# Optimization experiments

Measured on AMD Instinct MI355X. Metric: run time of the kernel, lower is better.

Reference implementation:

```python
import jax, jax.numpy as jnp
import numpy as np

N = 8192      # number of nodes (x is [N, N])
S = 2         # number of support (adjacency) matrices
E = 262144    # edges (nnz) per support, avg degree 32
D = 128       # output_dim


def setup_inputs() -> dict:
    key = jax.random.key(0)
    k0, k1, k2, k3, k4 = jax.random.split(key, 5)
    x = jax.random.normal(k0, (N, N), dtype=jnp.float32)
    rows = jax.random.randint(k1, (S, E), 0, N, dtype=jnp.int32)
    cols = jax.random.randint(k2, (S, E), 0, N, dtype=jnp.int32)
    vals = jax.random.uniform(k3, (S, E), dtype=jnp.float32)
    # one glorot [1, D] weight per support; stacked as [S, 1, D]
    w = jax.random.normal(k4, (S, 1, D), dtype=jnp.float32) * 0.05
    return {"x": x, "rows": rows, "cols": cols, "vals": vals, "w": w}


def reference(x, rows, cols, vals, w):
    # x = tf.abs(tf.transpose(x) - x * -1)  ==  |x^T + x|
    x2 = jnp.abs(x.T + x)                      # [N, N]
    # diag(A_s @ x2)[i] = sum_{(i,j) in E_s} A_s[i,j] * x2[j, i]
    contrib = vals * x2[cols, rows]            # [S, E] gather along edges
    diag = jax.vmap(
        lambda r, c: jax.ops.segment_sum(c, r, num_segments=N)
    )(rows, contrib)                           # [S, N]
    # outer product with per-support [1, D] weight, summed over supports
    out = jnp.einsum('sn,sd->nd', diag, w[:, 0, :])  # [N, D]
    return jax.nn.relu(out)
```

## Files before the change

kernel.cpp:

```cpp
#include <hip/hip_runtime.h>


#define N_NODES 8192
#define S_SUP   2
#define E_EDGES 262144
#define D_OUT   128

__global__ void gc_edge_kernel(const float* __restrict__ x,
                               const int*   __restrict__ rows,
                               const int*   __restrict__ cols,
                               const float* __restrict__ vals,
                               float*       __restrict__ diag) {
    int idx = blockIdx.x * blockDim.x + threadIdx.x;
    if (idx >= S_SUP * E_EDGES) return;
    int s = idx >> 18;
    int r = rows[idx];
    int c = cols[idx];
    float v = vals[idx];
    float a = x[(size_t)r * N_NODES + c];
    float b = x[(size_t)c * N_NODES + r];
    float t = fabsf(a + b) * v;
    atomicAdd(&diag[s * N_NODES + r], t);
}

__global__ void gc_out_kernel(const float* __restrict__ diag,
                              const float* __restrict__ w,
                              float*       __restrict__ out) {
    int idx = blockIdx.x * blockDim.x + threadIdx.x;
    int d4 = idx & (D_OUT / 4 - 1);
    int n  = idx >> 5;
    if (n >= N_NODES) return;
    float d0 = diag[n];
    float d1 = diag[N_NODES + n];
    const float4 w0 = ((const float4*)w)[d4];
    const float4 w1 = ((const float4*)w)[D_OUT / 4 + d4];
    float4 o;
    o.x = fmaxf(fmaf(d0, w0.x, d1 * w1.x), 0.0f);
    o.y = fmaxf(fmaf(d0, w0.y, d1 * w1.y), 0.0f);
    o.z = fmaxf(fmaf(d0, w0.z, d1 * w1.z), 0.0f);
    o.w = fmaxf(fmaf(d0, w0.w, d1 * w1.w), 0.0f);
    ((float4*)out)[idx] = o;
}

extern "C" void kernel_launch(void* const* d_in, const int* in_sizes, int n_in,
                              void* d_out, int out_size, void* d_ws, size_t ws_size,
                              hipStream_t stream) {
    const float* x    = (const float*)d_in[0];
    const int*   rows = (const int*)  d_in[1];
    const int*   cols = (const int*)  d_in[2];
    const float* vals = (const float*)d_in[3];
    const float* w    = (const float*)d_in[4];
    float* out  = (float*)d_out;
    float* diag = (float*)d_ws;

    hipMemsetAsync(diag, 0, (size_t)S_SUP * N_NODES * sizeof(float), stream);

    {
        int total = S_SUP * E_EDGES;
        int block = 256;
        int grid  = (total + block - 1) / block;
        gc_edge_kernel<<<grid, block, 0, stream>>>(x, rows, cols, vals, diag);
    }
    {
        int total = N_NODES * D_OUT / 4;
        int block = 256;
        int grid  = (total + block - 1) / block;
        gc_out_kernel<<<grid, block, 0, stream>>>(diag, w, out);
    }
}
```

Before: 44.05 us.

## Vectorize edge loads, process four edges per thread, replicate diag accumulators

Result: slower. 47.24 us (+7.2%).

```diff
diff --git a/kernel.cpp b/kernel.cpp
--- a/kernel.cpp
+++ b/kernel.cpp
@@ -5,33 +5,57 @@
 #define S_SUP   2
 #define E_EDGES 262144
 #define D_OUT   128
+#define NREP    4
 
-__global__ void gc_edge_kernel(const float* __restrict__ x,
-                               const int*   __restrict__ rows,
-                               const int*   __restrict__ cols,
-                               const float* __restrict__ vals,
-                               float*       __restrict__ diag) {
-    int idx = blockIdx.x * blockDim.x + threadIdx.x;
-    if (idx >= S_SUP * E_EDGES) return;
-    int s = idx >> 18;
-    int r = rows[idx];
-    int c = cols[idx];
-    float v = vals[idx];
-    float a = x[(size_t)r * N_NODES + c];
-    float b = x[(size_t)c * N_NODES + r];
-    float t = fabsf(a + b) * v;
-    atomicAdd(&diag[s * N_NODES + r], t);
+__global__ __launch_bounds__(256)
+void gc_edge4_kernel(const float* __restrict__ x,
+                     const int4*  __restrict__ rows4,
+                     const int4*  __restrict__ cols4,
+                     const float4* __restrict__ vals4,
+                     float*       __restrict__ diag,
+                     int rep_mask) {
+    int t = blockIdx.x * blockDim.x + threadIdx.x;
+    if (t >= S_SUP * E_EDGES / 4) return;
+    int4  r = rows4[t];
+    int4  c = cols4[t];
+    float4 v = vals4[t];
+    int s = t >> 16;
+
+    float a0 = x[(r.x << 13) | c.x];
+    float b0 = x[(c.x << 13) | r.x];
+    float a1 = x[(r.y << 13) | c.y];
+    float b1 = x[(c.y << 13) | r.y];
+    float a2 = x[(r.z << 13) | c.z];
+    float b2 = x[(c.z << 13) | r.z];
+    float a3 = x[(r.w << 13) | c.w];
+    float b3 = x[(c.w << 13) | r.w];
+
+    float t0 = fabsf(a0 + b0) * v.x;
+    float t1 = fabsf(a1 + b1) * v.y;
+    float t2 = fabsf(a2 + b2) * v.z;
+    float t3 = fabsf(a3 + b3) * v.w;
+
+    float* base = diag + (((blockIdx.x & rep_mask) * S_SUP + s) << 13);
+    atomicAdd(&base[r.x], t0);
+    atomicAdd(&base[r.y], t1);
+    atomicAdd(&base[r.z], t2);
+    atomicAdd(&base[r.w], t3);
 }
 
-__global__ void gc_out_kernel(const float* __restrict__ diag,
-                              const float* __restrict__ w,
-                              float*       __restrict__ out) {
+__global__ __launch_bounds__(256)
+void gc_out_kernel(const float* __restrict__ diag,
+                   const float* __restrict__ w,
+                   float*       __restrict__ out,
+                   int nrep) {
     int idx = blockIdx.x * blockDim.x + threadIdx.x;
     int d4 = idx & (D_OUT / 4 - 1);
     int n  = idx >> 5;
     if (n >= N_NODES) return;
-    float d0 = diag[n];
-    float d1 = diag[N_NODES + n];
+    float d0 = 0.0f, d1 = 0.0f;
+    for (int rp = 0; rp < nrep; ++rp) {
+        d0 += diag[((rp * S_SUP + 0) << 13) + n];
+        d1 += diag[((rp * S_SUP + 1) << 13) + n];
+    }
     const float4 w0 = ((const float4*)w)[d4];
     const float4 w1 = ((const float4*)w)[D_OUT / 4 + d4];
     float4 o;
@@ -53,18 +77,24 @@
     float* out  = (float*)d_out;
     float* diag = (float*)d_ws;
 
-    hipMemsetAsync(diag, 0, (size_t)S_SUP * N_NODES * sizeof(float), stream);
+    size_t per_rep = (size_t)S_SUP * N_NODES * sizeof(float);
+    int nrep = (ws_size >= NREP * per_rep) ? NREP : 1;
+    int rep_mask = nrep - 1;
+
+    hipMemsetAsync(diag, 0, (size_t)nrep * per_rep, stream);
 
     {
-        int total = S_SUP * E_EDGES;
+        int total = S_SUP * E_EDGES / 4;
         int block = 256;
         int grid  = (total + block - 1) / block;
-        gc_edge_kernel<<<grid, block, 0, stream>>>(x, rows, cols, vals, diag);
+        gc_edge4_kernel<<<grid, block, 0, stream>>>(
+            x, (const int4*)rows, (const int4*)cols, (const float4*)vals,
+            diag, rep_mask);
     }
     {
         int total = N_NODES * D_OUT / 4;
         int block = 256;
         int grid  = (total + block - 1) / block;
-        gc_out_kernel<<<grid, block, 0, stream>>>(diag, w, out);
+        gc_out_kernel<<<grid, block, 0, stream>>>(diag, w, out, nrep);
     }
 }
```
